# Kernel tuning notes

Hardware: AMD Instinct MI355X
Metric: run time of the kernel (lower is better)

Reference implementation:

```python
import jax, jax.numpy as jnp
import numpy as np

N, D, H, O, E = 4096, 1024, 4096, 1024, 8
TOP_K = 2

def setup_inputs() -> dict:
    key = jax.random.key(0)
    k = jax.random.split(key, 4)
    x  = jax.random.normal(k[0], (N, D), dtype=jnp.float32)
    Wg = jax.random.normal(k[1], (D, E), dtype=jnp.float32) * (1.0 / np.sqrt(D))
    W1 = jax.random.normal(k[2], (E, D, H), dtype=jnp.float32) * (1.0 / np.sqrt(D))
    b1 = jnp.zeros((E, H), dtype=jnp.float32)
    W2 = jax.random.normal(k[3], (E, H, O), dtype=jnp.float32) * (1.0 / np.sqrt(H))
    b2 = jnp.zeros((E, O), dtype=jnp.float32)
    return {"x": x, "Wg": Wg, "W1": W1, "b1": b1, "W2": W2, "b2": b2}

def reference(x, Wg, W1, b1, W2, b2):
    # Gate: Linear(bias=False) -> ReLU (lin() appends act) -> softmax
    logits = jax.nn.relu(x @ Wg)                      # [N, E]
    probs = jax.nn.softmax(logits, axis=1)            # [N, E]
    top_p, sel = jax.lax.top_k(probs, TOP_K)          # [N, K]
    top_p = top_p / jnp.sum(top_p, axis=-1, keepdims=True)
    # Per-token combine weights over experts: [N, E]
    combine = jnp.sum(jax.nn.one_hot(sel, E, dtype=x.dtype) * top_p[..., None], axis=1)
    # Experts: ReLU(x W1 + b1) -> ReLU(h W2 + b2); final ReLU because lin() adds act on output layer
    h = jax.nn.relu(jnp.einsum('nd,edh->enh', x, W1) + b1[:, None, :])   # [E, N, H]
    y = jax.nn.relu(jnp.einsum('enh,eho->eno', h, W2) + b2[:, None, :])  # [E, N, O]
    out = jnp.einsum('eno,ne->no', y, combine)                            # [N, O]
    return out
```

## Files before the change

### kernel.cpp

```cpp
#include <hip/hip_runtime.h>
#include <cstdint>

#define NTOK 4096
#define DDIM 1024
#define HDIM 4096
#define ODIM 1024
#define NEXP 8
#define NSLOT (2*NTOK)
#define MAXT128 72
#define MAXT256 40

typedef __bf16 bf16x8 __attribute__((ext_vector_type(8)));
typedef float  f32x4  __attribute__((ext_vector_type(4)));
typedef unsigned short ushort8v __attribute__((ext_vector_type(8)));

__device__ __forceinline__ unsigned short f2bf(float f) {
    union { float f; unsigned int u; } v; v.f = f;
    unsigned int r = (v.u + 0x7FFF + ((v.u >> 16) & 1)) >> 16;
    return (unsigned short)r;
}

typedef const void __attribute__((address_space(1)))* gas_ptr;
typedef void       __attribute__((address_space(3)))* las_ptr;

__global__ void gate_kernel(const float* __restrict__ x, const float* __restrict__ Wg,
                            int2* __restrict__ sel, float2* __restrict__ wts,
                            int* __restrict__ counts, unsigned short* __restrict__ xb) {
    int wave = threadIdx.x >> 6;
    int lane = threadIdx.x & 63;
    int n = blockIdx.x * 4 + wave;
    float acc[NEXP];
#pragma unroll
    for (int e = 0; e < NEXP; e++) acc[e] = 0.f;
    const float* xr = x + (size_t)n * DDIM;
    unsigned short* xbr = xb + (size_t)n * DDIM;
#pragma unroll
    for (int i = 0; i < 4; i++) {
        int d = i * 256 + lane * 4;
        float4 xv = *(const float4*)&xr[d];
        ushort4 o;
        o.x = f2bf(xv.x); o.y = f2bf(xv.y); o.z = f2bf(xv.z); o.w = f2bf(xv.w);
        *(ushort4*)&xbr[d] = o;
        const float* wr = Wg + (size_t)d * NEXP;
#pragma unroll
        for (int jj = 0; jj < 4; jj++) {
            float xs = (jj == 0) ? xv.x : (jj == 1) ? xv.y : (jj == 2) ? xv.z : xv.w;
#pragma unroll
            for (int e = 0; e < NEXP; e++)
                acc[e] = fmaf(xs, wr[jj * NEXP + e], acc[e]);
        }
    }
#pragma unroll
    for (int e = 0; e < NEXP; e++) {
#pragma unroll
        for (int off = 32; off >= 1; off >>= 1)
            acc[e] += __shfl_xor(acc[e], off, 64);
    }
    if (lane == 0) {
        float l0 = -1e30f, l1 = -1e30f; int e0 = 0, e1 = 0;
#pragma unroll
        for (int e = 0; e < NEXP; e++) {
            float v = fmaxf(acc[e], 0.f);
            if (v > l0)      { l1 = l0; e1 = e0; l0 = v; e0 = e; }
            else if (v > l1) { l1 = v;  e1 = e; }
        }
        float w0 = 1.f / (1.f + expf(l1 - l0));
        sel[n] = make_int2(e0, e1);
        wts[n] = make_float2(w0, 1.f - w0);
        atomicAdd(&counts[e0], 1);
        atomicAdd(&counts[e1], 1);
    }
}

__global__ void route_kernel(const int2* __restrict__ sel, const float2* __restrict__ wts,
                             const int* __restrict__ counts, int* __restrict__ offsets,
                             int4* __restrict__ t128, int* __restrict__ nt128,
                             int4* __restrict__ t256, int* __restrict__ nt256,
                             int* __restrict__ slot_token, float* __restrict__ slot_weight) {
    __shared__ int cur[NEXP];
    int t = threadIdx.x;
    if (t == 0) {
        int s = 0, n1 = 0, n2 = 0;
        for (int e = 0; e < NEXP; e++) {
            offsets[e] = s; cur[e] = s;
            int c = counts[e];
            for (int r = 0; r < c; r += 128)
                t128[n1++] = make_int4(e, s + r, min(128, c - r), 0);
            for (int r = 0; r < c; r += 256)
                t256[n2++] = make_int4(e, s + r, min(256, c - r), 0);
            s += c;
        }
        offsets[NEXP] = s;
        *nt128 = n1; *nt256 = n2;
    }
    __syncthreads();
    for (int n = t; n < NTOK; n += blockDim.x) {
        int2 se = sel[n]; float2 w = wts[n];
        int p0 = atomicAdd(&cur[se.x], 1);
        slot_token[p0] = n; slot_weight[p0] = w.x;
        int p1 = atomicAdd(&cur[se.y], 1);
        slot_token[p1] = n; slot_weight[p1] = w.y;
    }
}

__global__ void transpose_cast_kernel(const float* __restrict__ src, unsigned short* __restrict__ dst,
                                      int R, int C) {
    __shared__ float tile[64][65];
    int e = blockIdx.z;
    const float* s = src + (size_t)e * R * C;
    unsigned short* d = dst + (size_t)e * R * C;
    int t = threadIdx.x;
    int r0 = blockIdx.y * 64, c0 = blockIdx.x * 64;
#pragma unroll
    for (int p = 0; p < 4; p++) {
        int r = p * 16 + (t >> 4);
        int c = (t & 15) * 4;
        float4 v = *(const float4*)&s[(size_t)(r0 + r) * C + (c0 + c)];
        tile[r][c] = v.x; tile[r][c + 1] = v.y; tile[r][c + 2] = v.z; tile[r][c + 3] = v.w;
    }
    __syncthreads();
    int c = t >> 2, rb = (t & 3) * 16;
#pragma unroll
    for (int j = 0; j < 2; j++) {
        ushort8v v;
#pragma unroll
        for (int i = 0; i < 8; i++) v[i] = f2bf(tile[rb + j * 8 + i][c]);
        *(ushort8v*)&d[(size_t)(c0 + c) * R + (r0 + rb + j * 8)] = v;
    }
}

template <int MODE, int KDIM, int NDIM, int TM, int TN, int WMv>
__global__ __launch_bounds__(256, 2) void moe_gemm_kernel(
    const unsigned short* __restrict__ A,
    const unsigned short* __restrict__ B,
    const float* __restrict__ bias,
    const int4* __restrict__ tile_meta,
    const int* __restrict__ ntiles,
    const int* __restrict__ slot_token,
    const float* __restrict__ slot_weight,
    unsigned short* __restrict__ h,
    float* __restrict__ out) {

    int tileIdx, colBase;
    if constexpr (MODE == 1) {
        tileIdx = blockIdx.y;
        colBase = blockIdx.x * TN;
    } else {
        int j = blockIdx.y;
        tileIdx = blockIdx.x + 8 * (j >> 3);
        colBase = (j & 7) * TN;
    }
    if (tileIdx >= *ntiles) return;
    int4 tm = tile_meta[tileIdx];
    int e = tm.x, slotBase = tm.y, rows = tm.z;

    constexpr int RA = TM / 4, IA = RA / 16;
    constexpr int RB = TN / 4, IB = RB / 16;
    constexpr int NI = KDIM / 32;

    __shared__ __align__(16) unsigned short As[2][TM * 32];
    __shared__ __align__(16) unsigned short Bs[2][TN * 32];

    int tid = threadIdx.x;
    int w = tid >> 6, l = tid & 63;
    int quad = l >> 4, lr = l & 15;
    int wm = w % WMv, wn = w / WMv;

    int rl = l >> 2;
    int g = (l & 3) ^ ((l >> 3) & 3);

    const unsigned short* ag[IA];
    const unsigned short* bg[IB];
    const unsigned short* Be = B + (size_t)e * NDIM * KDIM;
#pragma unroll
    for (int j = 0; j < IA; j++) {
        int r = w * RA + j * 16 + rl;
        int slot = min(slotBase + r, NSLOT - 1);
        if constexpr (MODE == 1) {
            int tok = slot_token[slot];
            ag[j] = A + (size_t)tok * KDIM + g * 8;
        } else {
            ag[j] = A + (size_t)slot * KDIM + g * 8;
        }
    }
#pragma unroll
    for (int j = 0; j < IB; j++) {
        int r = w * RB + j * 16 + rl;
        bg[j] = Be + (size_t)(colBase + r) * KDIM + g * 8;
    }

    f32x4 zero = {0.f, 0.f, 0.f, 0.f};
    f32x4 acc[8][4];
#pragma unroll
    for (int m = 0; m < 8; m++)
#pragma unroll
        for (int n = 0; n < 4; n++) acc[m][n] = zero;

    int su = (quad ^ ((lr >> 1) & 3)) * 16;

    auto issue = [&](int k, int s) {
        unsigned short* AsW = &As[s][w * RA * 32];
        unsigned short* BsW = &Bs[s][w * RB * 32];
#pragma unroll
        for (int j = 0; j < IA; j++)
            __builtin_amdgcn_global_load_lds((gas_ptr)(ag[j] + k * 32), (las_ptr)(AsW + j * 512), 16, 0, 0);
#pragma unroll
        for (int j = 0; j < IB; j++)
            __builtin_amdgcn_global_load_lds((gas_ptr)(bg[j] + k * 32), (las_ptr)(BsW + j * 512), 16, 0, 0);
    };
    auto compute = [&](int s) {
        const char* A_ = (const char*)As[s];
        const char* B_ = (const char*)Bs[s];
        bf16x8 af[8], bf[4];
#pragma unroll
        for (int m = 0; m < 8; m++)
            af[m] = *(const bf16x8*)(A_ + (wm * 128 + m * 16 + lr) * 64 + su);
#pragma unroll
        for (int n = 0; n < 4; n++)
            bf[n] = *(const bf16x8*)(B_ + (wn * 64 + n * 16 + lr) * 64 + su);
#pragma unroll
        for (int m = 0; m < 8; m++)
#pragma unroll
            for (int n = 0; n < 4; n++)
                acc[m][n] = __builtin_amdgcn_mfma_f32_16x16x32_bf16(af[m], bf[n], acc[m][n], 0, 0, 0);
    };

    issue(0, 0);
    for (int k = 0; k < NI - 1; k++) {
        issue(k + 1, (k + 1) & 1);
        asm volatile("s_waitcnt vmcnt(6)" ::: "memory");
        asm volatile("s_barrier" ::: "memory");
        compute(k & 1);
        asm volatile("s_barrier" ::: "memory");
    }
    asm volatile("s_waitcnt vmcnt(0)" ::: "memory");
    asm volatile("s_barrier" ::: "memory");
    compute((NI - 1) & 1);

    if constexpr (MODE == 1) {
        const float* bv = bias + e * NDIM;
#pragma unroll
        for (int n = 0; n < 4; n++) {
            int gc = colBase + wn * 64 + n * 16 + lr;
            float b = bv[gc];
#pragma unroll
            for (int m = 0; m < 8; m++) {
                int rloc = wm * 128 + m * 16 + quad * 4;
#pragma unroll
                for (int i = 0; i < 4; i++) {
                    int r = rloc + i;
                    if (r < rows) {
                        float v = fmaxf(acc[m][n][i] + b, 0.f);
                        h[(size_t)(slotBase + r) * NDIM + gc] = f2bf(v);
                    }
                }
            }
        }
    } else {
        const float* bv = bias + e * NDIM;
#pragma unroll
        for (int m = 0; m < 8; m++) {
            int rloc = wm * 128 + m * 16 + quad * 4;
#pragma unroll
            for (int i = 0; i < 4; i++) {
                int r = rloc + i;
                if (r >= rows) continue;
                int s = slotBase + r;
                int tok = slot_token[s];
                float wgt = slot_weight[s];
                float* orow = out + (size_t)tok * ODIM;
#pragma unroll
                for (int n = 0; n < 4; n++) {
                    int gc = colBase + wn * 64 + n * 16 + lr;
                    float v = fmaxf(acc[m][n][i] + bv[gc], 0.f) * wgt;
                    atomicAdd(&orow[gc], v);
                }
            }
        }
    }
}

extern "C" void kernel_launch(void* const* d_in, const int* in_sizes, int n_in,
                              void* d_out, int out_size, void* d_ws, size_t ws_size,
                              hipStream_t stream) {
    const float* x  = (const float*)d_in[0];
    const float* Wg = (const float*)d_in[1];
    const float* W1 = (const float*)d_in[2];
    const float* b1 = (const float*)d_in[3];
    const float* W2 = (const float*)d_in[4];
    const float* b2 = (const float*)d_in[5];
    float* out = (float*)d_out;

    char* ws = (char*)d_ws;
    int*    counts      = (int*)(ws + 0);
    int*    offsets     = (int*)(ws + 64);
    int*    nt128       = (int*)(ws + 128);
    int*    nt256       = (int*)(ws + 132);
    int4*   t128        = (int4*)(ws + 256);
    int4*   t256        = (int4*)(ws + 2048);
    int2*   sel         = (int2*)(ws + 4096);
    float2* wts         = (float2*)(ws + 36864);
    int*    slot_token  = (int*)(ws + 69632);
    float*  slot_weight = (float*)(ws + 102400);
    unsigned short* xb  = (unsigned short*)(ws + 2097152);
    unsigned short* W1T = (unsigned short*)(ws + 10485760);
    unsigned short* W2T = (unsigned short*)(ws + 77594624);
    unsigned short* hbf = (unsigned short*)(ws + 144703488);

    hipMemsetAsync(d_out, 0, (size_t)NTOK * ODIM * sizeof(float), stream);
    hipMemsetAsync(ws, 0, 256, stream);

    gate_kernel<<<NTOK / 4, 256, 0, stream>>>(x, Wg, sel, wts, counts, xb);
    route_kernel<<<1, 512, 0, stream>>>(sel, wts, counts, offsets, t128, nt128, t256, nt256,
                                        slot_token, slot_weight);

    transpose_cast_kernel<<<dim3(HDIM / 64, DDIM / 64, NEXP), 256, 0, stream>>>(W1, W1T, DDIM, HDIM);
    transpose_cast_kernel<<<dim3(ODIM / 64, HDIM / 64, NEXP), 256, 0, stream>>>(W2, W2T, HDIM, ODIM);

    moe_gemm_kernel<1, DDIM, HDIM, 128, 256, 1><<<dim3(HDIM / 256, MAXT128), 256, 0, stream>>>(
        xb, W1T, b1, t128, nt128, slot_token, slot_weight, hbf, nullptr);
    moe_gemm_kernel<2, HDIM, ODIM, 256, 128, 2><<<dim3(8, MAXT256), 256, 0, stream>>>(
        hbf, W2T, b2, t256, nt256, slot_token, slot_weight, nullptr, out);
}
```

Measured before the change: 773.1 us.

## Replace direct global-to-LDS double buffer with register-staged single-buffer pipeline

Drops the double-buffered global_load_lds path and instead loads A/B tiles into registers, writes them to a single LDS buffer, and prefetches two steps ahead. The aim is to halve LDS usage, which could allow more resident blocks, and to keep loads in flight across the compute phase. In exchange it adds register pressure and VGPR-to-LDS write instructions, plus two block barriers per K step, which may reduce overlap compared with the asynchronous direct-to-LDS loads.

Result: slower. 1.230 ms (+59.1%).

```diff
diff --git a/kernel.cpp b/kernel.cpp
--- a/kernel.cpp
+++ b/kernel.cpp
@@ -19,9 +19,6 @@
     unsigned int r = (v.u + 0x7FFF + ((v.u >> 16) & 1)) >> 16;
     return (unsigned short)r;
 }
-
-typedef const void __attribute__((address_space(1)))* gas_ptr;
-typedef void       __attribute__((address_space(3)))* las_ptr;
 
 __global__ void gate_kernel(const float* __restrict__ x, const float* __restrict__ Wg,
                             int2* __restrict__ sel, float2* __restrict__ wts,
@@ -154,39 +151,42 @@
     int4 tm = tile_meta[tileIdx];
     int e = tm.x, slotBase = tm.y, rows = tm.z;
 
-    constexpr int RA = TM / 4, IA = RA / 16;
-    constexpr int RB = TN / 4, IB = RB / 16;
+    constexpr int PA = TM / 64;
+    constexpr int PB = TN / 64;
     constexpr int NI = KDIM / 32;
 
-    __shared__ __align__(16) unsigned short As[2][TM * 32];
-    __shared__ __align__(16) unsigned short Bs[2][TN * 32];
+    __shared__ __align__(16) unsigned short As[TM * 32];
+    __shared__ __align__(16) unsigned short Bs[TN * 32];
 
     int tid = threadIdx.x;
     int w = tid >> 6, l = tid & 63;
     int quad = l >> 4, lr = l & 15;
     int wm = w % WMv, wn = w / WMv;
 
-    int rl = l >> 2;
-    int g = (l & 3) ^ ((l >> 3) & 3);
-
-    const unsigned short* ag[IA];
-    const unsigned short* bg[IB];
+    int rl = tid >> 2;
+    int u  = tid & 3;
+    int us = u ^ ((rl >> 1) & 3);
+
+    const unsigned short* aq[PA]; int wa[PA];
+    const unsigned short* bq[PB]; int wb[PB];
     const unsigned short* Be = B + (size_t)e * NDIM * KDIM;
 #pragma unroll
-    for (int j = 0; j < IA; j++) {
-        int r = w * RA + j * 16 + rl;
+    for (int p = 0; p < PA; p++) {
+        int r = p * 64 + rl;
         int slot = min(slotBase + r, NSLOT - 1);
         if constexpr (MODE == 1) {
             int tok = slot_token[slot];
-            ag[j] = A + (size_t)tok * KDIM + g * 8;
+            aq[p] = A + (size_t)tok * KDIM + u * 8;
         } else {
-            ag[j] = A + (size_t)slot * KDIM + g * 8;
-        }
-    }
-#pragma unroll
-    for (int j = 0; j < IB; j++) {
-        int r = w * RB + j * 16 + rl;
-        bg[j] = Be + (size_t)(colBase + r) * KDIM + g * 8;
+            aq[p] = A + (size_t)slot * KDIM + u * 8;
+        }
+        wa[p] = r * 64 + us * 16;
+    }
+#pragma unroll
+    for (int p = 0; p < PB; p++) {
+        int r = p * 64 + rl;
+        bq[p] = Be + (size_t)(colBase + r) * KDIM + u * 8;
+        wb[p] = r * 64 + us * 16;
     }
 
     f32x4 zero = {0.f, 0.f, 0.f, 0.f};
@@ -198,19 +198,22 @@
 
     int su = (quad ^ ((lr >> 1) & 3)) * 16;
 
-    auto issue = [&](int k, int s) {
-        unsigned short* AsW = &As[s][w * RA * 32];
-        unsigned short* BsW = &Bs[s][w * RB * 32];
-#pragma unroll
-        for (int j = 0; j < IA; j++)
-            __builtin_amdgcn_global_load_lds((gas_ptr)(ag[j] + k * 32), (las_ptr)(AsW + j * 512), 16, 0, 0);
-#pragma unroll
-        for (int j = 0; j < IB; j++)
-            __builtin_amdgcn_global_load_lds((gas_ptr)(bg[j] + k * 32), (las_ptr)(BsW + j * 512), 16, 0, 0);
+    uint4 ra[PA], rb[PB];
+    auto gload = [&](int k) {
+#pragma unroll
+        for (int p = 0; p < PA; p++) ra[p] = *(const uint4*)(aq[p] + k * 32);
+#pragma unroll
+        for (int p = 0; p < PB; p++) rb[p] = *(const uint4*)(bq[p] + k * 32);
     };
-    auto compute = [&](int s) {
-        const char* A_ = (const char*)As[s];
-        const char* B_ = (const char*)Bs[s];
+    auto dswrite = [&]() {
+#pragma unroll
+        for (int p = 0; p < PA; p++) *(uint4*)((char*)As + wa[p]) = ra[p];
+#pragma unroll
+        for (int p = 0; p < PB; p++) *(uint4*)((char*)Bs + wb[p]) = rb[p];
+    };
+    auto compute = [&]() {
+        const char* A_ = (const char*)As;
+        const char* B_ = (const char*)Bs;
         bf16x8 af[8], bf[4];
 #pragma unroll
         for (int m = 0; m < 8; m++)
@@ -225,17 +228,19 @@
                 acc[m][n] = __builtin_amdgcn_mfma_f32_16x16x32_bf16(af[m], bf[n], acc[m][n], 0, 0, 0);
     };
 
-    issue(0, 0);
-    for (int k = 0; k < NI - 1; k++) {
-        issue(k + 1, (k + 1) & 1);
-        asm volatile("s_waitcnt vmcnt(6)" ::: "memory");
-        asm volatile("s_barrier" ::: "memory");
-        compute(k & 1);
-        asm volatile("s_barrier" ::: "memory");
-    }
-    asm volatile("s_waitcnt vmcnt(0)" ::: "memory");
-    asm volatile("s_barrier" ::: "memory");
-    compute((NI - 1) & 1);
+    gload(0);
+    dswrite();
+    gload(1);
+    __syncthreads();
+    for (int k = 0; k < NI; k++) {
+        compute();
+        if (k < NI - 1) {
+            __syncthreads();
+            dswrite();
+            if (k + 2 < NI) gload(k + 2);
+            __syncthreads();
+        }
+    }
 
     if constexpr (MODE == 1) {
         const float* bv = bias + e * NDIM;
```
